# Kernel optimization log

Measured on AMD Instinct MI355X. Metric: run time of the kernel, lower is better.

## Reference

```python
import math
import jax, jax.numpy as jnp
import numpy as np

H = 256      # hidden_size
HEADS = 8
DK = H // HEADS
B = 32
DL = 290     # drug length
PL = 1000    # protein length


def _pe(length, d):
    # sinusoidal positional encoding, d even
    pos = jnp.arange(length, dtype=jnp.float32)[:, None]
    div = jnp.exp(jnp.arange(0, d, 2, dtype=jnp.float32) * (-math.log(10000.0) / d))
    ang = pos * div  # [L, d/2]
    pe = jnp.zeros((length, d), jnp.float32)
    pe = pe.at[:, 0::2].set(jnp.sin(ang)).at[:, 1::2].set(jnp.cos(ang))
    return pe


def setup_inputs() -> dict:
    key = jax.random.key(0)
    ks = iter(jax.random.split(key, 48))
    def lin(din, dout):
        return jax.random.normal(next(ks), (din, dout), jnp.float32) * 0.02, jnp.zeros((dout,), jnp.float32)
    inp = {}
    inp['drug'] = jax.random.normal(next(ks), (B, DL, H), jnp.float32)
    inp['protein'] = jax.random.normal(next(ks), (B, PL, H), jnp.float32)
    inp['scale_d'] = jnp.ones((1,), jnp.float32)
    inp['scale_p'] = jnp.ones((1,), jnp.float32)
    for name in ['q_d', 'k_p', 'v_p', 'q_p', 'k_d', 'v_d', 'out_d', 'out_p']:
        w, b = lin(H, H)
        inp['w_' + name] = w
        inp['b_' + name] = b
    inp['alpha'] = jnp.asarray(0.5, jnp.float32)
    for name in ['fc_dp', 'fc_pd']:
        w, b = lin(HEADS, H)
        inp['w_' + name] = w
        inp['b_' + name] = b
    for name in ['gd', 'gp']:
        w, b = lin(H, H)
        inp['w_' + name] = w
        inp['b_' + name] = b
    return inp


def _split_heads(x):
    b, l, _ = x.shape
    return x.reshape(b, l, HEADS, DK).transpose(0, 2, 1, 3)  # [b, h, l, dk]


def _forward(drug, protein, scale_d, scale_p,
             w_q_d, b_q_d, w_k_p, b_k_p, w_v_p, b_v_p,
             w_q_p, b_q_p, w_k_d, b_k_d, w_v_d, b_v_d,
             alpha, w_out_d, b_out_d, w_out_p, b_out_p,
             w_fc_dp, b_fc_dp, w_fc_pd, b_fc_pd,
             w_gd, b_gd, w_gp, b_gp):
    b, dl, h = drug.shape
    pl = protein.shape[1]
    # positional encoding (buffers, non-learned except scale)
    drug_e = drug + scale_d * _pe(dl, h)
    prot_e = protein + scale_p * _pe(pl, h)

    Qd = _split_heads(drug_e @ w_q_d + b_q_d)   # [b,h,dl,dk]
    Kp = _split_heads(prot_e @ w_k_p + b_k_p)   # [b,h,pl,dk]
    Vp = _split_heads(prot_e @ w_v_p + b_v_p)
    Qp = _split_heads(prot_e @ w_q_p + b_q_p)
    Kd = _split_heads(drug_e @ w_k_d + b_k_d)
    Vd = _split_heads(drug_e @ w_v_d + b_v_d)

    inv_sqrt = 1.0 / math.sqrt(DK)
    attn_dp = jnp.einsum('bhid,bhjd->bhij', Qd, Kp) * inv_sqrt      # [b,h,dl,pl]
    # (Q_p K_d^T)^T along last two dims -> [b,h,dl,pl]
    attn_pd = jnp.einsum('bhjd,bhid->bhij', Qp, Kd) * inv_sqrt
    a = jax.nn.sigmoid(alpha)
    A = jax.nn.softmax(a * attn_dp + (1.0 - a) * attn_pd, axis=-1)  # [b,h,dl,pl]

    ctx_d = jnp.einsum('bhij,bhjd->bhid', A, Vp)  # [b,h,dl,dk]
    ctx_p = jnp.einsum('bhij,bhid->bhjd', A, Vd)  # [b,h,pl,dk]
    ctx_d = ctx_d.transpose(0, 2, 1, 3).reshape(b, dl, h) @ w_out_d + b_out_d
    ctx_p = ctx_p.transpose(0, 2, 1, 3).reshape(b, pl, h) @ w_out_p + b_out_p

    attn_dp_m = jnp.mean(A, axis=-1).transpose(0, 2, 1)   # [b,dl,heads]
    drug_attn = attn_dp_m @ w_fc_dp + b_fc_dp             # [b,dl,h]
    attn_pd_m = jnp.mean(A, axis=-2).transpose(0, 2, 1)   # [b,pl,heads]
    prot_attn = attn_pd_m @ w_fc_pd + b_fc_pd             # [b,pl,h]

    drug_gate = jax.nn.sigmoid(drug_e @ w_gd + b_gd)
    prot_gate = jax.nn.sigmoid(prot_e @ w_gp + b_gp)
    ctx_d = ctx_d * drug_gate
    ctx_p = ctx_p * prot_gate

    drug_upd = drug_e + ctx_d * jax.nn.sigmoid(drug_attn)
    prot_upd = prot_e + ctx_p * jax.nn.sigmoid(prot_attn)
    return jnp.concatenate([drug_upd, prot_upd], axis=1)  # [b, dl+pl, h]


def reference(drug, protein, scale_d, scale_p,
              w_q_d, b_q_d, w_k_p, b_k_p, w_v_p, b_v_p,
              w_q_p, b_q_p, w_k_d, b_k_d, w_v_d, b_v_d,
              alpha, w_out_d, b_out_d, w_out_p, b_out_p,
              w_fc_dp, b_fc_dp, w_fc_pd, b_fc_pd,
              w_gd, b_gd, w_gp, b_gp):
    return _forward(drug, protein, scale_d, scale_p,
                    w_q_d, b_q_d, w_k_p, b_k_p, w_v_p, b_v_p,
                    w_q_p, b_q_p, w_k_d, b_k_d, w_v_d, b_v_d,
                    alpha, w_out_d, b_out_d, w_out_p, b_out_p,
                    w_fc_dp, b_fc_dp, w_fc_pd, b_fc_pd,
                    w_gd, b_gd, w_gp, b_gp)
```

## Files before the change

kernel.cpp:

```cpp
#include <hip/hip_runtime.h>
#include <math.h>

typedef __attribute__((ext_vector_type(8))) short bf16x8;
typedef __attribute__((ext_vector_type(4))) float f32x4;
typedef unsigned short u16;
typedef unsigned int u32;

#define DEVFN static __device__ __forceinline__

constexpr int NB  = 32;
constexpr int DLn = 290;
constexpr int PLc = 1000;
constexpr int MD  = NB * DLn;
constexpr int MP  = NB * PLc;
constexpr int NSTRIP = 645;
constexpr int SPLIT  = 145;
constexpr int SG     = 81;

DEVFN u16 f2b(float f) {
    u32 u = __builtin_bit_cast(u32, f);
    u32 r = u + 0x7fffu + ((u >> 16) & 1u);
    return (u16)(r >> 16);
}
DEVFN float b2f(u16 s) { return __builtin_bit_cast(float, (u32)s << 16); }
DEVFN float sigm(float x) { return 1.0f / (1.0f + __expf(-x)); }
DEVFN int sw(int row, int col, int stride) { return row * stride + (col ^ ((row & 7) << 3)); }

__global__ void pe_kernel(float* __restrict__ pe) {
    int p = blockIdx.x, c = threadIdx.x;
    float div = __expf((float)(c & ~1) * (-9.210340371976184f / 256.0f));
    float ang = (float)p * div;
    pe[p * 256 + c] = (c & 1) ? cosf(ang) : sinf(ang);
}

__global__ void fcprep_kernel(const float* __restrict__ w, const float* __restrict__ b,
                              float* __restrict__ dfc) {
    int c = threadIdx.x;
    float s = b[c];
    #pragma unroll
    for (int hh = 0; hh < 8; hh++) s += 0.001f * w[hh * 256 + c];
    dfc[c] = s;
}

__global__ __launch_bounds__(256) void eadd_kernel(
        const float* __restrict__ drug, const float* __restrict__ prot,
        const float* __restrict__ scale_d, const float* __restrict__ scale_p,
        const float* __restrict__ pe,
        u16* __restrict__ e_d, u16* __restrict__ e_p) {
    int idx = blockIdx.x * 256 + threadIdx.x;
    int r = idx >> 6, c4 = (idx & 63) * 4;
    if (r < MD) {
        int i = r % DLn;
        float s = scale_d[0];
        float4 dv = *(const float4*)&drug[(size_t)r * 256 + c4];
        float4 pv = *(const float4*)&pe[i * 256 + c4];
        u16 o[4];
        o[0] = f2b(dv.x + s * pv.x); o[1] = f2b(dv.y + s * pv.y);
        o[2] = f2b(dv.z + s * pv.z); o[3] = f2b(dv.w + s * pv.w);
        *(uint2*)&e_d[(size_t)r * 256 + c4] = *(uint2*)o;
    } else {
        int rr = r - MD;
        int j = rr % PLc;
        float s = scale_p[0];
        float4 dv = *(const float4*)&prot[(size_t)rr * 256 + c4];
        float4 pv = *(const float4*)&pe[j * 256 + c4];
        u16 o[4];
        o[0] = f2b(dv.x + s * pv.x); o[1] = f2b(dv.y + s * pv.y);
        o[2] = f2b(dv.z + s * pv.z); o[3] = f2b(dv.w + s * pv.w);
        *(uint2*)&e_p[(size_t)rr * 256 + c4] = *(uint2*)o;
    }
}

struct WPtrs { const float* w[10]; };
__global__ __launch_bounds__(256) void wprep_kernel(WPtrs wp, u16* __restrict__ wt) {
    __shared__ u16 t[64][66];
    int m = blockIdx.y, tile = blockIdx.x;
    int k0 = (tile >> 2) * 64, n0 = (tile & 3) * 64;
    const float* w = wp.w[m];
    int r = threadIdx.x >> 6, c = threadIdx.x & 63;
    #pragma unroll
    for (int q = 0; q < 16; q++) {
        int rr = r + q * 4;
        t[rr][c] = f2b(w[(size_t)(k0 + rr) * 256 + n0 + c]);
    }
    __syncthreads();
    #pragma unroll
    for (int q = 0; q < 16; q++) {
        int rr = r + q * 4;
        wt[((size_t)m << 16) + (size_t)(n0 + rr) * 256 + k0 + c] = t[c][rr];
    }
}

struct PM { const u16* BT; const float* bias; u16* C; int sig; };
struct PCfg {
    const u16* Ab;
    PM m[4];
};
struct PCfg2 {
    PCfg c0, c1;
    const float* x0; const float* x1;
    const u16* gate0; const u16* gate1;
    const float* cm;
    const float* dfc;
    const float* wfc1; const float* bfc1;
    const float* scale0; const float* scale1;
    const float* pe;
    float* out;
};

template<int NM>
__global__ __launch_bounds__(256) void proj_kernel(PCfg2 cfgs) {
    const int d = blockIdx.x;
    const int x = d & 7, q = d >> 3;
    const int u  = (NM == 4) ? (q & 15) : (q & 3);
    const int sg = (NM == 4) ? (q >> 4) : (q >> 2);
    const int s = sg * 8 + x;
    if (s >= NSTRIP) return;
    const int mi = (NM == 4) ? (u >> 2) : 0;
    const int nt = (NM == 4) ? (u & 3) : u;
    const bool f1 = s < SPLIT;
    const int mt = f1 ? s : s - SPLIT;

    const u16* Ab   = f1 ? cfgs.c0.Ab : cfgs.c1.Ab;
    const u16*   BT   = f1 ? (mi==0?cfgs.c0.m[0].BT  :mi==1?cfgs.c0.m[1].BT  :mi==2?cfgs.c0.m[2].BT  :cfgs.c0.m[3].BT)
                           : (mi==0?cfgs.c1.m[0].BT  :mi==1?cfgs.c1.m[1].BT  :mi==2?cfgs.c1.m[2].BT  :cfgs.c1.m[3].BT);
    const float* bias = f1 ? (mi==0?cfgs.c0.m[0].bias:mi==1?cfgs.c0.m[1].bias:mi==2?cfgs.c0.m[2].bias:cfgs.c0.m[3].bias)
                           : (mi==0?cfgs.c1.m[0].bias:mi==1?cfgs.c1.m[1].bias:mi==2?cfgs.c1.m[2].bias:cfgs.c1.m[3].bias);
    u16*         C    = f1 ? (mi==0?cfgs.c0.m[0].C   :mi==1?cfgs.c0.m[1].C   :mi==2?cfgs.c0.m[2].C   :cfgs.c0.m[3].C)
                           : (mi==0?cfgs.c1.m[0].C   :mi==1?cfgs.c1.m[1].C   :mi==2?cfgs.c1.m[2].C   :cfgs.c1.m[3].C);
    const int    sig  = f1 ? (mi==0?cfgs.c0.m[0].sig :mi==1?cfgs.c0.m[1].sig :mi==2?cfgs.c0.m[2].sig :cfgs.c0.m[3].sig)
                           : (mi==0?cfgs.c1.m[0].sig :mi==1?cfgs.c1.m[1].sig :mi==2?cfgs.c1.m[2].sig :cfgs.c1.m[3].sig);

    __shared__ u16 Bs[64 * 256];
    __shared__ float fcb[(NM == 1) ? 2304 : 4];
    const int tid = threadIdx.x;
    const int lane = tid & 63, w = tid >> 6, ln = lane & 15, g = lane >> 4;

    const int lr = tid >> 2, lc = tid & 3;
    const int nur = ((lr >> 5) & 1) * 32 + ((lr >> 2) & 3) * 8 + ((lr >> 4) & 1) * 4 + (lr & 3);
    const u16* Bp = BT + (size_t)(nt * 64 + nur) * 256 + lc * 8;
    uint4 bv[8];
    #pragma unroll
    for (int kk = 0; kk < 8; kk++) bv[kk] = *(const uint4*)(Bp + kk * 32);

    const int row = mt * 64 + w * 16 + ln;
    bf16x8 Af[8];
    {
        const u16* Ap = Ab + (size_t)row * 256 + g * 8;
        #pragma unroll
        for (int ks = 0; ks < 8; ks++)
            Af[ks] = *(const bf16x8*)(Ap + ks * 32);
    }

    if (NM == 1 && !f1) {
        *(float4*)&fcb[tid * 8]     = *(const float4*)&cfgs.wfc1[tid * 8];
        *(float4*)&fcb[tid * 8 + 4] = *(const float4*)&cfgs.wfc1[tid * 8 + 4];
        fcb[2048 + tid] = cfgs.bfc1[tid];
    }

    #pragma unroll
    for (int kk = 0; kk < 8; kk++)
        *(uint4*)&Bs[sw(lr, lc * 8 + kk * 32, 256)] = bv[kk];
    __syncthreads();

    f32x4 acc[4] = {};
    #pragma unroll
    for (int ks = 0; ks < 8; ks++) {
        #pragma unroll
        for (int ntl = 0; ntl < 4; ntl++) {
            bf16x8 bf = *(const bf16x8*)&Bs[sw(ntl * 16 + ln, ks * 32 + g * 8, 256)];
            acc[ntl] = __builtin_amdgcn_mfma_f32_16x16x32_bf16(bf, Af[ks], acc[ntl], 0, 0, 0);
        }
    }

    const int base0 = nt * 64 + g * 8, base1 = base0 + 32;
    f32x4 b0 = *(const f32x4*)&bias[base0];
    f32x4 b1 = *(const f32x4*)&bias[base0 + 4];
    f32x4 b2 = *(const f32x4*)&bias[base1];
    f32x4 b3 = *(const f32x4*)&bias[base1 + 4];
    float v[16];
    #pragma unroll
    for (int t = 0; t < 4; t++) {
        v[t]      = acc[0][t] + b0[t];
        v[4 + t]  = acc[1][t] + b1[t];
        v[8 + t]  = acc[2][t] + b2[t];
        v[12 + t] = acc[3][t] + b3[t];
    }
    if (NM == 4) {
        if (sig) {
            #pragma unroll
            for (int t = 0; t < 16; t++) v[t] = sigm(v[t]);
        }
        u16 o[16];
        #pragma unroll
        for (int t = 0; t < 16; t++) o[t] = f2b(v[t]);
        u16* Cp = C + (size_t)row * 256;
        *(uint4*)&Cp[base0] = *(uint4*)&o[0];
        *(uint4*)&Cp[base1] = *(uint4*)&o[8];
    } else {
        (void)C; (void)sig;
        const float* X     = f1 ? cfgs.x0 : cfgs.x1;
        const u16* gate    = f1 ? cfgs.gate0 : cfgs.gate1;
        const float* scale = f1 ? cfgs.scale0 : cfgs.scale1;
        const float* pe    = cfgs.pe;
        const float sc = scale[0];
        const int pos  = f1 ? (row % DLn) : (row % PLc);
        const int bidx = f1 ? (row / DLn) : (row / PLc);
        const int orow = bidx * 1290 + (f1 ? pos : 290 + pos);
        float aw[16];
        if (f1) {
            const float* dfc = cfgs.dfc;
            *(float4*)&aw[0]  = *(const float4*)&dfc[base0];
            *(float4*)&aw[4]  = *(const float4*)&dfc[base0 + 4];
            *(float4*)&aw[8]  = *(const float4*)&dfc[base1];
            *(float4*)&aw[12] = *(const float4*)&dfc[base1 + 4];
        } else {
            float cmv[8];
            float4 ca = *(const float4*)&cfgs.cm[(size_t)row * 8];
            float4 cb = *(const float4*)&cfgs.cm[(size_t)row * 8 + 4];
            cmv[0]=ca.x; cmv[1]=ca.y; cmv[2]=ca.z; cmv[3]=ca.w;
            cmv[4]=cb.x; cmv[5]=cb.y; cmv[6]=cb.z; cmv[7]=cb.w;
            #pragma unroll
            for (int t = 0; t < 16; t++) {
                const int col = (t < 8) ? (base0 + t) : (base1 + t - 8);
                float s2 = fcb[2048 + col];
                #pragma unroll
                for (int hh = 0; hh < 8; hh++) s2 += cmv[hh] * fcb[hh * 256 + col];
                aw[t] = s2;
            }
        }
        u16 ge[16];
        *(uint4*)&ge[0] = *(const uint4*)&gate[(size_t)row * 256 + base0];
        *(uint4*)&ge[8] = *(const uint4*)&gate[(size_t)row * 256 + base1];
        float outv[16];
        #pragma unroll
        for (int half = 0; half < 2; half++) {
            const int cb0 = half ? base1 : base0;
            #pragma unroll
            for (int t4 = 0; t4 < 2; t4++) {
                float4 xa = *(const float4*)&X[(size_t)row * 256 + cb0 + t4 * 4];
                float4 pa = *(const float4*)&pe[(size_t)pos * 256 + cb0 + t4 * 4];
                #pragma unroll
                for (int t = 0; t < 4; t++) {
                    const int idx = half * 8 + t4 * 4 + t;
                    float e = (&xa.x)[t] + sc * (&pa.x)[t];
                    outv[idx] = e + v[idx] * b2f(ge[idx]) * sigm(aw[idx]);
                }
            }
        }
        float* Op = cfgs.out + (size_t)orow * 256;
        *(float4*)&Op[base0]     = *(float4*)&outv[0];
        *(float4*)&Op[base0 + 4] = *(float4*)&outv[4];
        *(float4*)&Op[base1]     = *(float4*)&outv[8];
        *(float4*)&Op[base1 + 4] = *(float4*)&outv[12];
    }
}

__global__ __launch_bounds__(512) void attn_kernel(
        const u16* __restrict__ Qd, const u16* __restrict__ Kd, const u16* __restrict__ Vd,
        const u16* __restrict__ Kp, const u16* __restrict__ Vp, const u16* __restrict__ Qp,
        const float* __restrict__ alpha,
        u16* __restrict__ ctx_d, u16* __restrict__ ctx_p, float* __restrict__ cm) {
    __shared__ u16 Ks[2][64 * 64];
    __shared__ union {
        struct { u16 VpT[2][32 * 64]; u16 Pm[320 * 64]; } s1;
        struct { u16 PT[64 * 320]; u16 VdT[32 * 320]; } s2;
    } U;
    __shared__ float r_l[320];
    __shared__ float colpart[8][64];

    const int bh = blockIdx.x, b = bh >> 3, h = bh & 7;
    const int tid = threadIdx.x;
    const int w = tid >> 6, lane = tid & 63, ln = lane & 15, g = lane >> 4;

    const float a = sigm(alpha[0]);
    const float inv = 0.1767766952966369f;
    const float sa = a * inv, sb = (1.0f - a) * inv;
    const int nmt = (w < 4) ? 3 : 2;
    const int mtsA[3] = { w, w + 8, w + 16 };

    const size_t rbd = (size_t)b * DLn * 256 + h * 32;
    const size_t rbp = (size_t)b * PLc * 256 + h * 32;

    bf16x8 Qf[3][2];
    #pragma unroll
    for (int t = 0; t < 3; t++) {
        const int i = mtsA[t] * 16 + ln;
        #pragma unroll
        for (int ks = 0; ks < 2; ks++) {
            u16 o[8] = {0,0,0,0,0,0,0,0};
            if (t < nmt && i < DLn) {
                const u16* src = (ks ? Kd : Qd) + rbd + (size_t)i * 256 + g * 8;
                const float s = ks ? sb : sa;
                uint4 v = *(const uint4*)src;
                u16 e[8]; *(uint4*)e = v;
                #pragma unroll
                for (int q = 0; q < 8; q++) o[q] = f2b(b2f(e[q]) * s);
            }
            Qf[t][ks] = *(bf16x8*)o;
        }
    }

    const int s_jj = tid >> 3, s_ch = tid & 7;
    const u16* s_src = ((s_ch >> 2) ? Qp : Kp) + rbp + (s_ch & 3) * 8;
    const int v_j = tid & 63, v_d0 = (tid >> 6) * 4;

    {
        int j = s_jj;
        uint4 kv = (j < PLc) ? *(const uint4*)(s_src + (size_t)j * 256) : make_uint4(0,0,0,0);
        uint2 vv = (v_j < PLc) ? *(const uint2*)(Vp + rbp + (size_t)v_j * 256 + v_d0) : make_uint2(0,0);
        *(uint4*)&Ks[0][sw(s_jj, s_ch * 8, 64)] = kv;
        u16 e[4]; *(uint2*)e = vv;
        #pragma unroll
        for (int q = 0; q < 4; q++) U.s1.VpT[0][sw(v_d0 + q, v_j, 64)] = e[q];
    }
    __syncthreads();

    float rs[3] = {0.f, 0.f, 0.f};
    f32x4 accd[3][2] = {};
    for (int jt = 0; jt < 16; jt++) {
        const int cur = jt & 1, j0 = jt * 64;
        const int jn = j0 + 64 + s_jj;
        uint4 kv = (jn < PLc) ? *(const uint4*)(s_src + (size_t)jn * 256) : make_uint4(0,0,0,0);
        const int vn = j0 + 64 + v_j;
        uint2 vv = (vn < PLc) ? *(const uint2*)(Vp + rbp + (size_t)vn * 256 + v_d0) : make_uint2(0,0);

        bf16x8 kf[4][2];
        #pragma unroll
        for (int js = 0; js < 4; js++)
            #pragma unroll
            for (int ks = 0; ks < 2; ks++)
                kf[js][ks] = *(const bf16x8*)&Ks[cur][sw(js * 16 + ln, ks * 32 + g * 8, 64)];

        #pragma unroll
        for (int t = 0; t < 3; t++) {
            if (t >= nmt) break;
            const int mt = mtsA[t];
            f32x4 acc[4] = {};
            #pragma unroll
            for (int ks = 0; ks < 2; ks++)
                #pragma unroll
                for (int js = 0; js < 4; js++)
                    acc[js] = __builtin_amdgcn_mfma_f32_16x16x32_bf16(kf[js][ks], Qf[t][ks], acc[js], 0, 0, 0);
            const int irow = mt * 16 + ln;
            #pragma unroll
            for (int js = 0; js < 4; js++) {
                u16 pb[4];
                float psum = 0.f;
                #pragma unroll
                for (int r = 0; r < 4; r++) {
                    float p = __expf(acc[js][r]);
                    psum += p;
                    pb[r] = f2b(p);
                }
                rs[t] += psum;
                *(ushort4*)&U.s1.Pm[sw(irow, js * 16 + g * 4, 64)] = *(ushort4*)pb;
            }
        }
        #pragma unroll
        for (int t = 0; t < 3; t++) {
            if (t >= nmt) break;
            const int mt = mtsA[t];
            #pragma unroll
            for (int ks2 = 0; ks2 < 2; ks2++) {
                bf16x8 af = *(const bf16x8*)&U.s1.Pm[sw(mt * 16 + ln, ks2 * 32 + g * 8, 64)];
                #pragma unroll
                for (int nd = 0; nd < 2; nd++) {
                    bf16x8 bv = *(const bf16x8*)&U.s1.VpT[cur][sw(nd * 16 + ln, ks2 * 32 + g * 8, 64)];
                    accd[t][nd] = __builtin_amdgcn_mfma_f32_16x16x32_bf16(bv, af, accd[t][nd], 0, 0, 0);
                }
            }
        }
        *(uint4*)&Ks[cur ^ 1][sw(s_jj, s_ch * 8, 64)] = kv;
        {
            u16 e[4]; *(uint2*)e = vv;
            #pragma unroll
            for (int q = 0; q < 4; q++) U.s1.VpT[cur ^ 1][sw(v_d0 + q, v_j, 64)] = e[q];
        }
        __syncthreads();
    }

    #pragma unroll
    for (int t = 0; t < 3; t++) {
        float v = rs[t];
        v += __shfl_xor(v, 16);
        v += __shfl_xor(v, 32);
        rs[t] = v;
    }
    if (g == 0) {
        #pragma unroll
        for (int t = 0; t < 3; t++) {
            if (t >= nmt) break;
            const int i = mtsA[t] * 16 + ln;
            r_l[i] = (i < DLn) ? 1.0f / (rs[t] - 24.0f) : 0.0f;
        }
    }
    __syncthreads();

    #pragma unroll
    for (int t = 0; t < 3; t++) {
        if (t >= nmt) break;
        const int i = mtsA[t] * 16 + ln;
        if (i < DLn) {
            const float ri = r_l[i];
            #pragma unroll
            for (int nd = 0; nd < 2; nd++) {
                u16 o[4];
                #pragma unroll
                for (int r = 0; r < 4; r++) o[r] = f2b(accd[t][nd][r] * ri);
                *(uint2*)&ctx_d[rbd + (size_t)i * 256 + nd * 16 + g * 4] = *(uint2*)o;
            }
        }
    }
    for (int c = tid; c < 320 * 8; c += 512) {
        const int i = c >> 3, d0 = (c & 7) * 4;
        u16 o[4] = {0,0,0,0};
        if (i < DLn) {
            const float ri = r_l[i];
            uint2 v = *(const uint2*)(Vd + rbd + (size_t)i * 256 + d0);
            u16 e[4]; *(uint2*)e = v;
            #pragma unroll
            for (int q = 0; q < 4; q++) o[q] = f2b(b2f(e[q]) * ri);
        }
        #pragma unroll
        for (int q = 0; q < 4; q++) U.s2.VdT[sw(d0 + q, i, 320)] = o[q];
    }
    {
        int j = s_jj;
        uint4 kv = (j < PLc) ? *(const uint4*)(s_src + (size_t)j * 256) : make_uint4(0,0,0,0);
        *(uint4*)&Ks[0][sw(s_jj, s_ch * 8, 64)] = kv;
    }
    float rr[3][4];
    #pragma unroll
    for (int t = 0; t < 3; t++)
        #pragma unroll
        for (int r = 0; r < 4; r++)
            rr[t][r] = (t < nmt) ? r_l[mtsA[t] * 16 + g * 4 + r] : 0.0f;
    __syncthreads();

    for (int jt = 0; jt < 16; jt++) {
        const int cur = jt & 1, j0 = jt * 64;
        const int jn = j0 + 64 + s_jj;
        uint4 kv = (jn < PLc) ? *(const uint4*)(s_src + (size_t)jn * 256) : make_uint4(0,0,0,0);

        bf16x8 kf[4][2];
        #pragma unroll
        for (int js = 0; js < 4; js++)
            #pragma unroll
            for (int ks = 0; ks < 2; ks++)
                kf[js][ks] = *(const bf16x8*)&Ks[cur][sw(js * 16 + ln, ks * 32 + g * 8, 64)];

        float csl[4] = {0.f, 0.f, 0.f, 0.f};
        #pragma unroll
        for (int t = 0; t < 3; t++) {
            if (t >= nmt) break;
            const int mt = mtsA[t];
            f32x4 acc[4] = {};
            #pragma unroll
            for (int ks = 0; ks < 2; ks++)
                #pragma unroll
                for (int js = 0; js < 4; js++)
                    acc[js] = __builtin_amdgcn_mfma_f32_16x16x32_bf16(Qf[t][ks], kf[js][ks], acc[js], 0, 0, 0);
            #pragma unroll
            for (int js = 0; js < 4; js++) {
                u16 pb[4];
                #pragma unroll
                for (int r = 0; r < 4; r++) {
                    float p = __expf(acc[js][r]);
                    csl[js] += p * rr[t][r];
                    pb[r] = f2b(p);
                }
                *(ushort4*)&U.s2.PT[sw(js * 16 + ln, mt * 16 + g * 4, 320)] = *(ushort4*)pb;
            }
        }
        #pragma unroll
        for (int js = 0; js < 4; js++) {
            float v = csl[js];
            v += __shfl_xor(v, 16);
            v += __shfl_xor(v, 32);
            csl[js] = v;
        }
        if (g == 0) {
            #pragma unroll
            for (int js = 0; js < 4; js++) colpart[w][js * 16 + ln] = csl[js];
        }
        *(uint4*)&Ks[cur ^ 1][sw(s_jj, s_ch * 8, 64)] = kv;
        __syncthreads();

        {
            const int js2 = w & 3, ds2 = w >> 2;
            f32x4 ap = {};
            #pragma unroll
            for (int k = 0; k < 10; k++) {
                bf16x8 af = *(const bf16x8*)&U.s2.PT[sw(js2 * 16 + ln, k * 32 + g * 8, 320)];
                bf16x8 bv = *(const bf16x8*)&U.s2.VdT[sw(ds2 * 16 + ln, k * 32 + g * 8, 320)];
                ap = __builtin_amdgcn_mfma_f32_16x16x32_bf16(bv, af, ap, 0, 0, 0);
            }
            const int j = j0 + js2 * 16 + ln;
            if (j < PLc) {
                u16 o[4];
                #pragma unroll
                for (int r = 0; r < 4; r++) o[r] = f2b(ap[r]);
                *(uint2*)&ctx_p[rbp + (size_t)j * 256 + ds2 * 16 + g * 4] = *(uint2*)o;
            }
        }
        if (w == 0) {
            float tot = 0.f;
            #pragma unroll
            for (int ww = 0; ww < 8; ww++) tot += colpart[ww][lane];
            const int j = j0 + lane;
            if (j < PLc) cm[(size_t)(b * PLc + j) * 8 + h] = tot * (1.0f / 290.0f);
        }
        __syncthreads();
    }
}

extern "C" void kernel_launch(void* const* d_in, const int* in_sizes, int n_in,
                              void* d_out, int out_size, void* d_ws, size_t ws_size,
                              hipStream_t stream) {
    (void)in_sizes; (void)n_in; (void)out_size;
    const float* drug    = (const float*)d_in[0];
    const float* prot    = (const float*)d_in[1];
    const float* scale_d = (const float*)d_in[2];
    const float* scale_p = (const float*)d_in[3];

    char* ws = (char*)d_ws;
    size_t off = 0;
    auto alloc = [&](size_t bytes) -> void* {
        void* p = ws + off;
        off += (bytes + 255) & ~(size_t)255;
        return p;
    };
    float* pe   = (float*)alloc((size_t)1000 * 256 * 4);
    u16* wt     = (u16*)alloc((size_t)10 * 65536 * 2);
    u16* e_d    = (u16*)alloc((size_t)MD * 256 * 2);
    u16* e_p    = (u16*)alloc((size_t)MP * 256 * 2);
    u16* Qd     = (u16*)alloc((size_t)MD * 256 * 2);
    u16* Kd     = (u16*)alloc((size_t)MD * 256 * 2);
    u16* Vd     = (u16*)alloc((size_t)MD * 256 * 2);
    u16* gate_d = (u16*)alloc((size_t)MD * 256 * 2);
    u16* Kp     = (u16*)alloc((size_t)MP * 256 * 2);
    u16* Vp     = (u16*)alloc((size_t)MP * 256 * 2);
    u16* Qp     = (u16*)alloc((size_t)MP * 256 * 2);
    u16* gate_p = (u16*)alloc((size_t)MP * 256 * 2);
    u16* ctxd   = (u16*)alloc((size_t)MD * 256 * 2);
    u16* ctxp   = (u16*)alloc((size_t)MP * 256 * 2);
    float* cm   = (float*)alloc((size_t)MP * 8 * 4);
    float* dfc  = (float*)alloc((size_t)256 * 4);
    if (off > ws_size) return;

    pe_kernel<<<1000, 256, 0, stream>>>(pe);
    fcprep_kernel<<<1, 256, 0, stream>>>((const float*)d_in[21], (const float*)d_in[22], dfc);

    WPtrs wp;
    const int wsrc[10] = {4, 12, 14, 25, 6, 8, 10, 27, 16, 18};
    for (int m = 0; m < 10; m++) wp.w[m] = (const float*)d_in[wsrc[m]];
    wprep_kernel<<<dim3(16, 10), 256, 0, stream>>>(wp, wt);

    eadd_kernel<<<(MD + MP) / 4, 256, 0, stream>>>(drug, prot, scale_d, scale_p, pe, e_d, e_p);

    auto W = [&](int slot) { return wt + (size_t)slot * 65536; };

    PCfg2 p1 = {};
    p1.c0 = { e_d,
              { { W(0), (const float*)d_in[5],  Qd,     0 },
                { W(1), (const float*)d_in[13], Kd,     0 },
                { W(2), (const float*)d_in[15], Vd,     0 },
                { W(3), (const float*)d_in[26], gate_d, 1 } } };
    p1.c1 = { e_p,
              { { W(4), (const float*)d_in[7],  Kp,     0 },
                { W(5), (const float*)d_in[9],  Vp,     0 },
                { W(6), (const float*)d_in[11], Qp,     0 },
                { W(7), (const float*)d_in[28], gate_p, 1 } } };
    proj_kernel<4><<<SG * 8 * 16, 256, 0, stream>>>(p1);

    attn_kernel<<<256, 512, 0, stream>>>(Qd, Kd, Vd, Kp, Vp, Qp,
                                         (const float*)d_in[20], ctxd, ctxp, cm);

    PCfg2 p2 = {};
    p2.c0 = { ctxd, { { W(8), (const float*)d_in[17], nullptr, 0 }, {}, {}, {} } };
    p2.c1 = { ctxp, { { W(9), (const float*)d_in[19], nullptr, 0 }, {}, {}, {} } };
    p2.x0 = drug;  p2.x1 = prot;
    p2.gate0 = gate_d;  p2.gate1 = gate_p;
    p2.cm = cm;
    p2.dfc = dfc;
    p2.wfc1 = (const float*)d_in[23];  p2.bfc1 = (const float*)d_in[24];
    p2.scale0 = scale_d;  p2.scale1 = scale_p;
    p2.pe = pe;
    p2.out = (float*)d_out;
    proj_kernel<1><<<SG * 8 * 4, 256, 0, stream>>>(p2);
}
```

Baseline: 185.3 us.

## Fuse positional-encoding add into projection kernel and use exp2 in attention

```diff
diff --git a/kernel.cpp b/kernel.cpp
--- a/kernel.cpp
+++ b/kernel.cpp
@@ -40,35 +40,6 @@
     #pragma unroll
     for (int hh = 0; hh < 8; hh++) s += 0.001f * w[hh * 256 + c];
     dfc[c] = s;
-}
-
-__global__ __launch_bounds__(256) void eadd_kernel(
-        const float* __restrict__ drug, const float* __restrict__ prot,
-        const float* __restrict__ scale_d, const float* __restrict__ scale_p,
-        const float* __restrict__ pe,
-        u16* __restrict__ e_d, u16* __restrict__ e_p) {
-    int idx = blockIdx.x * 256 + threadIdx.x;
-    int r = idx >> 6, c4 = (idx & 63) * 4;
-    if (r < MD) {
-        int i = r % DLn;
-        float s = scale_d[0];
-        float4 dv = *(const float4*)&drug[(size_t)r * 256 + c4];
-        float4 pv = *(const float4*)&pe[i * 256 + c4];
-        u16 o[4];
-        o[0] = f2b(dv.x + s * pv.x); o[1] = f2b(dv.y + s * pv.y);
-        o[2] = f2b(dv.z + s * pv.z); o[3] = f2b(dv.w + s * pv.w);
-        *(uint2*)&e_d[(size_t)r * 256 + c4] = *(uint2*)o;
-    } else {
-        int rr = r - MD;
-        int j = rr % PLc;
-        float s = scale_p[0];
-        float4 dv = *(const float4*)&prot[(size_t)rr * 256 + c4];
-        float4 pv = *(const float4*)&pe[j * 256 + c4];
-        u16 o[4];
-        o[0] = f2b(dv.x + s * pv.x); o[1] = f2b(dv.y + s * pv.y);
-        o[2] = f2b(dv.z + s * pv.z); o[3] = f2b(dv.w + s * pv.w);
-        *(uint2*)&e_p[(size_t)rr * 256 + c4] = *(uint2*)o;
-    }
 }
 
 struct WPtrs { const float* w[10]; };
@@ -145,7 +116,27 @@
 
     const int row = mt * 64 + w * 16 + ln;
     bf16x8 Af[8];
-    {
+    if (NM == 4) {
+        const float* X     = f1 ? cfgs.x0 : cfgs.x1;
+        const float* scale = f1 ? cfgs.scale0 : cfgs.scale1;
+        const int pos = f1 ? (row % DLn) : (row % PLc);
+        const float sc = scale[0];
+        const float* Xp_ = X + (size_t)row * 256 + g * 8;
+        const float* Pe_ = cfgs.pe + (size_t)pos * 256 + g * 8;
+        #pragma unroll
+        for (int ks = 0; ks < 8; ks++) {
+            float4 xa = *(const float4*)(Xp_ + ks * 32);
+            float4 xb = *(const float4*)(Xp_ + ks * 32 + 4);
+            float4 pa = *(const float4*)(Pe_ + ks * 32);
+            float4 pb = *(const float4*)(Pe_ + ks * 32 + 4);
+            u16 o[8];
+            o[0] = f2b(xa.x + sc * pa.x); o[1] = f2b(xa.y + sc * pa.y);
+            o[2] = f2b(xa.z + sc * pa.z); o[3] = f2b(xa.w + sc * pa.w);
+            o[4] = f2b(xb.x + sc * pb.x); o[5] = f2b(xb.y + sc * pb.y);
+            o[6] = f2b(xb.z + sc * pb.z); o[7] = f2b(xb.w + sc * pb.w);
+            Af[ks] = *(bf16x8*)o;
+        }
+    } else {
         const u16* Ap = Ab + (size_t)row * 256 + g * 8;
         #pragma unroll
         for (int ks = 0; ks < 8; ks++)
@@ -275,7 +266,8 @@
 
     const float a = sigm(alpha[0]);
     const float inv = 0.1767766952966369f;
-    const float sa = a * inv, sb = (1.0f - a) * inv;
+    const float l2e = 1.4426950408889634f;
+    const float sa = a * inv * l2e, sb = (1.0f - a) * inv * l2e;
     const int nmt = (w < 4) ? 3 : 2;
     const int mtsA[3] = { w, w + 8, w + 16 };
 
@@ -349,7 +341,7 @@
                 float psum = 0.f;
                 #pragma unroll
                 for (int r = 0; r < 4; r++) {
-                    float p = __expf(acc[js][r]);
+                    float p = exp2f(acc[js][r]);
                     psum += p;
                     pb[r] = f2b(p);
                 }
@@ -466,7 +458,7 @@
                 u16 pb[4];
                 #pragma unroll
                 for (int r = 0; r < 4; r++) {
-                    float p = __expf(acc[js][r]);
+                    float p = exp2f(acc[js][r]);
                     csl[js] += p * rr[t][r];
                     pb[r] = f2b(p);
                 }
@@ -533,8 +525,6 @@
     };
     float* pe   = (float*)alloc((size_t)1000 * 256 * 4);
     u16* wt     = (u16*)alloc((size_t)10 * 65536 * 2);
-    u16* e_d    = (u16*)alloc((size_t)MD * 256 * 2);
-    u16* e_p    = (u16*)alloc((size_t)MP * 256 * 2);
     u16* Qd     = (u16*)alloc((size_t)MD * 256 * 2);
     u16* Kd     = (u16*)alloc((size_t)MD * 256 * 2);
     u16* Vd     = (u16*)alloc((size_t)MD * 256 * 2);
@@ -557,21 +547,22 @@
     for (int m = 0; m < 10; m++) wp.w[m] = (const float*)d_in[wsrc[m]];
     wprep_kernel<<<dim3(16, 10), 256, 0, stream>>>(wp, wt);
 
-    eadd_kernel<<<(MD + MP) / 4, 256, 0, stream>>>(drug, prot, scale_d, scale_p, pe, e_d, e_p);
-
     auto W = [&](int slot) { return wt + (size_t)slot * 65536; };
 
     PCfg2 p1 = {};
-    p1.c0 = { e_d,
+    p1.c0 = { nullptr,
               { { W(0), (const float*)d_in[5],  Qd,     0 },
                 { W(1), (const float*)d_in[13], Kd,     0 },
                 { W(2), (const float*)d_in[15], Vd,     0 },
                 { W(3), (const float*)d_in[26], gate_d, 1 } } };
-    p1.c1 = { e_p,
+    p1.c1 = { nullptr,
               { { W(4), (const float*)d_in[7],  Kp,     0 },
                 { W(5), (const float*)d_in[9],  Vp,     0 },
                 { W(6), (const float*)d_in[11], Qp,     0 },
                 { W(7), (const float*)d_in[28], gate_p, 1 } } };
+    p1.x0 = drug;  p1.x1 = prot;
+    p1.scale0 = scale_d;  p1.scale1 = scale_p;
+    p1.pe = pe;
     proj_kernel<4><<<SG * 8 * 16, 256, 0, stream>>>(p1);
 
     attn_kernel<<<256, 512, 0, stream>>>(Qd, Kd, Vd, Kp, Vp, Qp,
```

After: 321.9 us. 73.7% more time.
